# Kernel optimization log

Hardware: AMD Instinct MI355X
Metric: run time of the kernel (lower is better)

The kernel has to match this reference:

```python
import jax, jax.numpy as jnp
import numpy as np

TEMP = 1.0  # routing_temperature

def _gelu(x):
    return jax.nn.gelu(x, approximate=False)  # torch nn.GELU default (erf)

def setup_inputs() -> dict:
    key = jax.random.key(0)
    ks = jax.random.split(key, 6)
    B, S, D, E, I = 8, 2048, 768, 8, 3072
    H = I // 2
    def xav(k, shape):
        fan_in, fan_out = shape[-2], shape[-1]
        lim = float(np.sqrt(6.0 / (fan_in + fan_out)))
        return jax.random.uniform(k, shape, jnp.float32, -lim, lim)
    return {
        "x":  jax.random.normal(ks[0], (B, S, D), jnp.float32),
        "Wr": xav(ks[1], (D, E)),
        "br": jnp.zeros((E,), jnp.float32),
        "W1": xav(ks[2], (E, D, I)), "b1": jnp.zeros((E, I), jnp.float32),
        "W2": xav(ks[3], (E, I, H)), "b2": jnp.zeros((E, H), jnp.float32),
        "W3": xav(ks[4], (E, H, D)), "b3": jnp.zeros((E, D), jnp.float32),
        "top_k": 2,
    }

def reference(x, Wr, br, W1, b1, W2, b2, W3, b3, top_k):
    B, S, D = x.shape
    E = Wr.shape[1]
    T = B * S
    xt = x.reshape(T, D)                              # flatten tokens
    logits = (xt @ Wr + br) / TEMP                    # [T, E]
    vals, sel = jax.lax.top_k(logits, top_k)          # [T, k]
    w = jax.nn.softmax(vals, axis=-1)                 # softmax over top-k scores
    # dense per-token combine weights (zero for unselected experts)
    combine = jnp.zeros((T, E), x.dtype).at[jnp.arange(T)[:, None], sel].add(w)
    def step(acc, p):
        W1e, b1e, W2e, b2e, W3e, b3e, ce = p
        h = _gelu(xt @ W1e + b1e)                     # [T, I]
        h = _gelu(h @ W2e + b2e)                      # [T, I//2]
        y = h @ W3e + b3e                             # [T, D]
        return acc + ce[:, None] * y, None
    acc0 = jnp.zeros((T, D), x.dtype)
    out, _ = jax.lax.scan(step, acc0, (W1, b1, W2, b2, W3, b3, combine.T))
    return out.reshape(B, S, D)
```

## Files before the change

kernel.cpp:

```cpp
#include <hip/hip_runtime.h>
#include <hip/hip_fp16.h>
#include <cstdint>
#include <cstddef>

#define TK 16384
#define DD 768
#define EE 8
#define II 3072
#define HH 1536

typedef _Float16 half8 __attribute__((ext_vector_type(8)));
typedef float floatx4 __attribute__((ext_vector_type(4)));

typedef const __attribute__((address_space(1))) uint32_t* gptr_t;
typedef __attribute__((address_space(3))) uint32_t* lptr_t;

#define GLOAD_LDS16(gp, lp) __builtin_amdgcn_global_load_lds( \
    (gptr_t)(const void*)(gp), (lptr_t)(void*)(lp), 16, 0, 0)

__device__ inline void xcd_swizzle(int& e, int& m, int& n) {
  int gx = gridDim.x, gy = gridDim.y;
  int f = (blockIdx.z * gy + blockIdx.y) * gx + blockIdx.x;
  int xcd = f & 7, idx = f >> 3;
  int chunk = idx / gx, pos = idx - chunk * gx;
  int logical = chunk * (8 * gx) + xcd * gx + pos;
  int mn = gy * gx;
  e = logical / mn;
  int rem = logical - e * mn;
  m = rem / gx;
  n = rem - m * gx;
}

__global__ __launch_bounds__(256)
void cvtT_kernel(const float* __restrict__ in, __half* __restrict__ out,
                 int K, int N) {
  __shared__ float tile[64][65];
  int e = blockIdx.z;
  const float* inp = in + (size_t)e * K * N + (size_t)(blockIdx.y * 64) * N + blockIdx.x * 64;
  __half* outp = out + (size_t)e * K * N + (size_t)(blockIdx.x * 64) * K + blockIdx.y * 64;
  int s = threadIdx.x;
  int tx = s & 15, r0 = s >> 4;
#pragma unroll
  for (int i = 0; i < 4; ++i) {
    int k = r0 + i * 16;
    float4 v = *(const float4*)&inp[(size_t)k * N + tx * 4];
    tile[k][tx * 4 + 0] = v.x;
    tile[k][tx * 4 + 1] = v.y;
    tile[k][tx * 4 + 2] = v.z;
    tile[k][tx * 4 + 3] = v.w;
  }
  __syncthreads();
  int kp = s & 31;
#pragma unroll
  for (int i = 0; i < 8; ++i) {
    int n = (s >> 5) + i * 8;
    __half2 h = __floats2half2_rn(tile[2 * kp][n], tile[2 * kp + 1][n]);
    *(__half2*)&outp[(size_t)n * K + kp * 2] = h;
  }
}

__global__ __launch_bounds__(256)
void router_kernel(const float* __restrict__ x, const float* __restrict__ Wr,
                   const float* __restrict__ br, int* __restrict__ counts,
                   int* __restrict__ sel, float* __restrict__ wTok,
                   __half* __restrict__ xh) {
  __shared__ float wr_s[EE * DD];
  for (int i = threadIdx.x; i < EE * DD; i += 256) {
    int d = i >> 3, e = i & 7;
    wr_s[e * DD + d] = Wr[i];
  }
  __syncthreads();
  int wid = threadIdx.x >> 6, lane = threadIdx.x & 63;
  int t = blockIdx.x * 4 + wid;
  const float* xt = x + (size_t)t * DD;
  float acc[EE];
#pragma unroll
  for (int e = 0; e < EE; ++e) acc[e] = 0.f;
  for (int d = lane; d < DD; d += 64) {
    float xv = xt[d];
#pragma unroll
    for (int e = 0; e < EE; ++e) acc[e] += xv * wr_s[e * DD + d];
  }
#pragma unroll
  for (int off = 32; off > 0; off >>= 1)
#pragma unroll
    for (int e = 0; e < EE; ++e) acc[e] += __shfl_xor(acc[e], off);
  if (lane == 0) {
    float v[EE];
#pragma unroll
    for (int e = 0; e < EE; ++e) v[e] = acc[e] + br[e];
    int i0 = 0;
#pragma unroll
    for (int e = 1; e < EE; ++e) if (v[e] > v[i0]) i0 = e;
    int i1 = (i0 == 0) ? 1 : 0;
#pragma unroll
    for (int e = 0; e < EE; ++e) if (e != i0 && v[e] > v[i1] && e != i1) { if (v[e] > v[i1]) i1 = e; }
    float e1 = __expf(v[i1] - v[i0]);
    float s = 1.f / (1.f + e1);
    sel[2 * t] = i0; sel[2 * t + 1] = i1;
    wTok[2 * t] = s; wTok[2 * t + 1] = e1 * s;
    atomicAdd(&counts[i0], 1);
    atomicAdd(&counts[i1], 1);
  }
  const float4* xr = (const float4*)xt;
  uint2* xo = (uint2*)(xh + (size_t)t * DD);
#pragma unroll
  for (int j = 0; j < 3; ++j) {
    float4 v = xr[lane + j * 64];
    __half2 a = __floats2half2_rn(v.x, v.y);
    __half2 b = __floats2half2_rn(v.z, v.w);
    uint2 p;
    p.x = *(const unsigned int*)&a;
    p.y = *(const unsigned int*)&b;
    xo[lane + j * 64] = p;
  }
}

__global__ void offsets_kernel(const int* __restrict__ counts, int* __restrict__ offsets,
                               int* __restrict__ cursors) {
  if (threadIdx.x == 0) {
    int o = 0;
    for (int e = 0; e < EE; ++e) { offsets[e] = o; cursors[e] = o; o += counts[e]; }
  }
}

__global__ void scatter_kernel(const int* __restrict__ sel, int* __restrict__ cursors,
                               int* __restrict__ idxList, int* __restrict__ posTok) {
  int t = blockIdx.x * 256 + threadIdx.x;
  if (t < TK) {
#pragma unroll
    for (int k = 0; k < 2; ++k) {
      int e = sel[2 * t + k];
      int p = atomicAdd(&cursors[e], 1);
      idxList[p] = t;
      posTok[2 * t + k] = p;
    }
  }
}

template<int KD, int ND, bool GATHER, bool GELU>
__global__ __launch_bounds__(512, 1)
void ffn_gemm8(const __half* __restrict__ A, const __half* __restrict__ Wt,
               const float* __restrict__ Bias, __half* __restrict__ Out,
               const int* __restrict__ counts, const int* __restrict__ offsets,
               const int* __restrict__ idxList) {
  constexpr int NT = KD / 64;
  int e, mblk, nblk;
  xcd_swizzle(e, mblk, nblk);
  const int cnt = counts[e];
  const int m0 = mblk * 256;
  if (cnt == 0 || m0 >= cnt) return;
  const int off = offsets[e];
  const int n0 = nblk * 256;
  const __half* We = Wt + (size_t)e * KD * ND;
  const float* be = Bias + (size_t)e * ND;

  __shared__ __align__(16) __half As[2][256 * 64];
  __shared__ __align__(16) __half Bs[2][256 * 64];

  const int tid = threadIdx.x;
  const int srow = tid >> 3;
  const int swz = ((tid & 7) ^ (srow & 7)) << 3;

  const __half* aptr[4];
  const __half* bptr[4];
#pragma unroll
  for (int q = 0; q < 4; ++q) {
    int gr = m0 + q * 64 + srow;
    if (gr > cnt - 1) gr = cnt - 1;
    size_t arow = GATHER ? (size_t)idxList[off + gr] : (size_t)(off + gr);
    aptr[q] = A + arow * KD + swz;
    bptr[q] = We + (size_t)(n0 + q * 64 + srow) * KD + swz;
  }

#define STAGE_A(BUF, Q, TS) GLOAD_LDS16(aptr[Q] + (TS) * 64, &As[BUF][(Q) * 4096 + tid * 8])
#define STAGE_B(BUF, Q, TS) GLOAD_LDS16(bptr[Q] + (TS) * 64, &Bs[BUF][(Q) * 4096 + tid * 8])

  const int lane = tid & 63, wv = tid >> 6;
  const int wr = wv >> 2, wc = wv & 3;
  const int lrow = lane & 15, lg = lane >> 4;
  const int rowa = wr * 128 + lrow;
  const int rowb = wc * 64 + lrow;
  int aoff[2], boff[2];
#pragma unroll
  for (int kk = 0; kk < 2; ++kk) {
    aoff[kk] = rowa * 64 + (((kk * 4 + lg) ^ (rowa & 7)) << 3);
    boff[kk] = rowb * 64 + (((kk * 4 + lg) ^ (rowb & 7)) << 3);
  }

  floatx4 acc[8][4];
#pragma unroll
  for (int mi = 0; mi < 8; ++mi)
#pragma unroll
    for (int ni = 0; ni < 4; ++ni) acc[mi][ni] = (floatx4){0.f, 0.f, 0.f, 0.f};

#pragma unroll
  for (int q = 0; q < 4; ++q) STAGE_A(0, q, 0);
#pragma unroll
  for (int q = 0; q < 4; ++q) STAGE_B(0, q, 0);
#pragma unroll
  for (int q = 0; q < 4; ++q) STAGE_A(1, q, 1);
  STAGE_B(1, 0, 1);
  STAGE_B(1, 1, 1);
  asm volatile("s_waitcnt vmcnt(6)" ::: "memory");
  __builtin_amdgcn_s_barrier();

#define BAR() __builtin_amdgcn_s_barrier()
#define WLG() do { asm volatile("s_waitcnt lgkmcnt(0)" ::: "memory"); \
                   __builtin_amdgcn_sched_barrier(0); } while (0)
#define P1() __builtin_amdgcn_s_setprio(1)
#define P0() __builtin_amdgcn_s_setprio(0)
#define MMQ(AF, BF, MB, NB) \
  _Pragma("unroll") for (int kk = 0; kk < 2; ++kk) \
  _Pragma("unroll") for (int mi = 0; mi < 4; ++mi) \
  _Pragma("unroll") for (int ni = 0; ni < 2; ++ni) \
    acc[(MB) + mi][(NB) + ni] = __builtin_amdgcn_mfma_f32_16x16x32_f16( \
        AF[mi][kk], BF[ni][kk], acc[(MB) + mi][(NB) + ni], 0, 0, 0);

#define PHASES(CUR, NXT, TT) { \
  const __half* Ac = &As[CUR][0]; \
  const __half* Bc = &Bs[CUR][0]; \
  half8 af[4][2], bf0[2][2], bf1[2][2]; \
  _Pragma("unroll") for (int mi = 0; mi < 4; ++mi) \
  _Pragma("unroll") for (int kk = 0; kk < 2; ++kk) \
    af[mi][kk] = *(const half8*)&Ac[aoff[kk] + mi * 1024]; \
  _Pragma("unroll") for (int ni = 0; ni < 2; ++ni) \
  _Pragma("unroll") for (int kk = 0; kk < 2; ++kk) \
    bf0[ni][kk] = *(const half8*)&Bc[boff[kk] + ni * 1024]; \
  if ((TT) + 1 < NT) { STAGE_B(NXT, 2, (TT) + 1); STAGE_B(NXT, 3, (TT) + 1); } \
  BAR(); WLG(); P1(); MMQ(af, bf0, 0, 0); P0(); BAR(); \
  _Pragma("unroll") for (int ni = 0; ni < 2; ++ni) \
  _Pragma("unroll") for (int kk = 0; kk < 2; ++kk) \
    bf1[ni][kk] = *(const half8*)&Bc[boff[kk] + (ni + 2) * 1024]; \
  if ((TT) + 2 < NT) { STAGE_A(CUR, 0, (TT) + 2); STAGE_A(CUR, 2, (TT) + 2); } \
  BAR(); WLG(); P1(); MMQ(af, bf1, 0, 2); P0(); BAR(); \
  _Pragma("unroll") for (int mi = 0; mi < 4; ++mi) \
  _Pragma("unroll") for (int kk = 0; kk < 2; ++kk) \
    af[mi][kk] = *(const half8*)&Ac[aoff[kk] + (mi + 4) * 1024]; \
  if ((TT) + 2 < NT) { STAGE_B(CUR, 0, (TT) + 2); STAGE_B(CUR, 1, (TT) + 2); } \
  BAR(); WLG(); P1(); MMQ(af, bf0, 4, 0); P0(); BAR(); \
  if ((TT) + 2 < NT) { STAGE_A(CUR, 1, (TT) + 2); STAGE_A(CUR, 3, (TT) + 2); } \
  BAR(); P1(); MMQ(af, bf1, 4, 2); P0(); \
  if ((TT) + 2 < NT) { asm volatile("s_waitcnt vmcnt(6)" ::: "memory"); } \
  else              { asm volatile("s_waitcnt vmcnt(0)" ::: "memory"); } \
  BAR(); }

  for (int t = 0; t < NT; t += 2) {
    PHASES(0, 1, t)
    PHASES(1, 0, t + 1)
  }

  const int crow = m0 + wr * 128 + lg * 4;
  const int ccol = n0 + wc * 64 + lrow;
  float bv[4];
#pragma unroll
  for (int ni = 0; ni < 4; ++ni) bv[ni] = be[ccol + ni * 16];
#pragma unroll
  for (int mi = 0; mi < 8; ++mi) {
#pragma unroll
    for (int j = 0; j < 4; ++j) {
      int r = crow + mi * 16 + j;
      if (r < cnt) {
#pragma unroll
        for (int ni = 0; ni < 4; ++ni) {
          float v = acc[mi][ni][j] + bv[ni];
          if (GELU) v = 0.5f * v * (1.f + erff(v * 0.70710678118654752f));
          Out[(size_t)(off + r) * ND + ccol + ni * 16] = __float2half(v);
        }
      }
    }
  }
#undef STAGE_A
#undef STAGE_B
#undef BAR
#undef WLG
#undef P1
#undef P0
#undef MMQ
#undef PHASES
}

__global__ void combine_kernel(const __half* __restrict__ yc, const float* __restrict__ wTok,
                               const int* __restrict__ posTok, float* __restrict__ out) {
  int t = blockIdx.x;
  int d = threadIdx.x * 4;
  if (d >= DD) return;
  float w0 = wTok[2 * t], w1 = wTok[2 * t + 1];
  const __half2* a = (const __half2*)(yc + (size_t)posTok[2 * t] * DD + d);
  const __half2* b = (const __half2*)(yc + (size_t)posTok[2 * t + 1] * DD + d);
  float2 a0 = __half22float2(a[0]), a1 = __half22float2(a[1]);
  float2 b0 = __half22float2(b[0]), b1 = __half22float2(b[1]);
  float4 r;
  r.x = w0 * a0.x + w1 * b0.x;
  r.y = w0 * a0.y + w1 * b0.y;
  r.z = w0 * a1.x + w1 * b1.x;
  r.w = w0 * a1.y + w1 * b1.y;
  *(float4*)(out + (size_t)t * DD + d) = r;
}

extern "C" void kernel_launch(void* const* d_in, const int* in_sizes, int n_in,
                              void* d_out, int out_size, void* d_ws, size_t ws_size,
                              hipStream_t stream) {
  const float* x  = (const float*)d_in[0];
  const float* Wr = (const float*)d_in[1];
  const float* br = (const float*)d_in[2];
  const float* W1 = (const float*)d_in[3];
  const float* b1 = (const float*)d_in[4];
  const float* W2 = (const float*)d_in[5];
  const float* b2 = (const float*)d_in[6];
  const float* W3 = (const float*)d_in[7];
  const float* b3 = (const float*)d_in[8];
  float* out = (float*)d_out;

  char* ws = (char*)d_ws;
  size_t o = 0;
  auto alloc = [&](size_t bytes) {
    char* p = ws + o;
    o += (bytes + 255) & ~(size_t)255;
    return p;
  };
  __half* xh   = (__half*)alloc((size_t)TK * DD * 2);
  __half* w1t  = (__half*)alloc((size_t)EE * DD * II * 2);
  __half* w2t  = (__half*)alloc((size_t)EE * II * HH * 2);
  __half* w3t  = (__half*)alloc((size_t)EE * HH * DD * 2);
  __half* h1   = (__half*)alloc((size_t)2 * TK * II * 2);
  __half* h2   = (__half*)alloc((size_t)2 * TK * HH * 2);
  __half* yc   = (__half*)alloc((size_t)2 * TK * DD * 2);
  int*   idxL  = (int*)alloc(2 * TK * 4);
  int*   sel   = (int*)alloc(2 * TK * 4);
  float* wTok  = (float*)alloc(2 * TK * 4);
  int*   posT  = (int*)alloc(2 * TK * 4);
  int*   counts  = (int*)alloc(256);
  int*   offsets = (int*)alloc(256);
  int*   cursors = (int*)alloc(256);
  if (o > ws_size) return;

  hipMemsetAsync(counts, 0, 256, stream);

  cvtT_kernel<<<dim3(II / 64, DD / 64, EE), 256, 0, stream>>>(W1, w1t, DD, II);
  cvtT_kernel<<<dim3(HH / 64, II / 64, EE), 256, 0, stream>>>(W2, w2t, II, HH);
  cvtT_kernel<<<dim3(DD / 64, HH / 64, EE), 256, 0, stream>>>(W3, w3t, HH, DD);
  router_kernel<<<TK / 4, 256, 0, stream>>>(x, Wr, br, counts, sel, wTok, xh);
  offsets_kernel<<<1, 64, 0, stream>>>(counts, offsets, cursors);
  scatter_kernel<<<TK / 256, 256, 0, stream>>>(sel, cursors, idxL, posT);

  ffn_gemm8<DD, II, true,  true ><<<dim3(II / 256, 64, EE), 512, 0, stream>>>(
      xh, w1t, b1, h1, counts, offsets, idxL);
  ffn_gemm8<II, HH, false, true ><<<dim3(HH / 256, 64, EE), 512, 0, stream>>>(
      h1, w2t, b2, h2, counts, offsets, idxL);
  ffn_gemm8<HH, DD, false, false><<<dim3(DD / 256, 64, EE), 512, 0, stream>>>(
      h2, w3t, b3, yc, counts, offsets, idxL);

  combine_kernel<<<TK, 192, 0, stream>>>(yc, wTok, posT, out);
}
```

Baseline: 1.505 ms.

## Load all A fragments up front and reverse block order in second GEMM

The GEMM phase schedule now reads all eight A fragments from LDS at the start of each k-tile rather than in two halves. Because of that, all four A stage loads for tile t+2 can be issued earlier, and one wait-and-barrier point is dropped. The second FFN GEMM also walks its blocks in reverse order, which may let it start on data the first GEMM just wrote while it is still in cache, and may balance the tail. The price is more registers for the A fragments under a 512-thread, 1-wave launch bound, which could cause spills.

```diff
diff --git a/kernel.cpp b/kernel.cpp
--- a/kernel.cpp
+++ b/kernel.cpp
@@ -18,9 +18,10 @@
 #define GLOAD_LDS16(gp, lp) __builtin_amdgcn_global_load_lds( \
     (gptr_t)(const void*)(gp), (lptr_t)(void*)(lp), 16, 0, 0)
 
-__device__ inline void xcd_swizzle(int& e, int& m, int& n) {
+__device__ inline void xcd_swizzle(int& e, int& m, int& n, bool rev) {
   int gx = gridDim.x, gy = gridDim.y;
   int f = (blockIdx.z * gy + blockIdx.y) * gx + blockIdx.x;
+  if (rev) f = gx * gy * 8 - 1 - f;
   int xcd = f & 7, idx = f >> 3;
   int chunk = idx / gx, pos = idx - chunk * gx;
   int logical = chunk * (8 * gx) + xcd * gx + pos;
@@ -138,7 +139,7 @@
   }
 }
 
-template<int KD, int ND, bool GATHER, bool GELU>
+template<int KD, int ND, bool GATHER, bool GELU, bool REV>
 __global__ __launch_bounds__(512, 1)
 void ffn_gemm8(const __half* __restrict__ A, const __half* __restrict__ Wt,
                const float* __restrict__ Bias, __half* __restrict__ Out,
@@ -146,7 +147,7 @@
                const int* __restrict__ idxList) {
   constexpr int NT = KD / 64;
   int e, mblk, nblk;
-  xcd_swizzle(e, mblk, nblk);
+  xcd_swizzle(e, mblk, nblk, REV);
   const int cnt = counts[e];
   const int m0 = mblk * 256;
   if (cnt == 0 || m0 >= cnt) return;
@@ -210,37 +211,38 @@
                    __builtin_amdgcn_sched_barrier(0); } while (0)
 #define P1() __builtin_amdgcn_s_setprio(1)
 #define P0() __builtin_amdgcn_s_setprio(0)
-#define MMQ(AF, BF, MB, NB) \
+#define MMQ(AO, BF, MB, NB) \
   _Pragma("unroll") for (int kk = 0; kk < 2; ++kk) \
   _Pragma("unroll") for (int mi = 0; mi < 4; ++mi) \
   _Pragma("unroll") for (int ni = 0; ni < 2; ++ni) \
     acc[(MB) + mi][(NB) + ni] = __builtin_amdgcn_mfma_f32_16x16x32_f16( \
-        AF[mi][kk], BF[ni][kk], acc[(MB) + mi][(NB) + ni], 0, 0, 0);
+        af[(AO) + mi][kk], BF[ni][kk], acc[(MB) + mi][(NB) + ni], 0, 0, 0);
 
 #define PHASES(CUR, NXT, TT) { \
   const __half* Ac = &As[CUR][0]; \
   const __half* Bc = &Bs[CUR][0]; \
-  half8 af[4][2], bf0[2][2], bf1[2][2]; \
-  _Pragma("unroll") for (int mi = 0; mi < 4; ++mi) \
+  half8 af[8][2], bf0[2][2], bf1[2][2]; \
+   \
+  _Pragma("unroll") for (int mi = 0; mi < 8; ++mi) \
   _Pragma("unroll") for (int kk = 0; kk < 2; ++kk) \
     af[mi][kk] = *(const half8*)&Ac[aoff[kk] + mi * 1024]; \
   _Pragma("unroll") for (int ni = 0; ni < 2; ++ni) \
   _Pragma("unroll") for (int kk = 0; kk < 2; ++kk) \
     bf0[ni][kk] = *(const half8*)&Bc[boff[kk] + ni * 1024]; \
   if ((TT) + 1 < NT) { STAGE_B(NXT, 2, (TT) + 1); STAGE_B(NXT, 3, (TT) + 1); } \
-  BAR(); WLG(); P1(); MMQ(af, bf0, 0, 0); P0(); BAR(); \
+  BAR(); WLG(); P1(); MMQ(0, bf0, 0, 0); P0(); BAR(); \
+   \
   _Pragma("unroll") for (int ni = 0; ni < 2; ++ni) \
   _Pragma("unroll") for (int kk = 0; kk < 2; ++kk) \
     bf1[ni][kk] = *(const half8*)&Bc[boff[kk] + (ni + 2) * 1024]; \
-  if ((TT) + 2 < NT) { STAGE_A(CUR, 0, (TT) + 2); STAGE_A(CUR, 2, (TT) + 2); } \
-  BAR(); WLG(); P1(); MMQ(af, bf1, 0, 2); P0(); BAR(); \
-  _Pragma("unroll") for (int mi = 0; mi < 4; ++mi) \
-  _Pragma("unroll") for (int kk = 0; kk < 2; ++kk) \
-    af[mi][kk] = *(const half8*)&Ac[aoff[kk] + (mi + 4) * 1024]; \
+  if ((TT) + 2 < NT) { STAGE_A(CUR, 0, (TT) + 2); STAGE_A(CUR, 1, (TT) + 2); \
+                       STAGE_A(CUR, 2, (TT) + 2); STAGE_A(CUR, 3, (TT) + 2); } \
+  BAR(); WLG(); P1(); MMQ(0, bf1, 0, 2); P0(); BAR(); \
+   \
   if ((TT) + 2 < NT) { STAGE_B(CUR, 0, (TT) + 2); STAGE_B(CUR, 1, (TT) + 2); } \
-  BAR(); WLG(); P1(); MMQ(af, bf0, 4, 0); P0(); BAR(); \
-  if ((TT) + 2 < NT) { STAGE_A(CUR, 1, (TT) + 2); STAGE_A(CUR, 3, (TT) + 2); } \
-  BAR(); P1(); MMQ(af, bf1, 4, 2); P0(); \
+  BAR(); P1(); MMQ(4, bf0, 4, 0); P0(); BAR(); \
+   \
+  P1(); MMQ(4, bf1, 4, 2); P0(); \
   if ((TT) + 2 < NT) { asm volatile("s_waitcnt vmcnt(6)" ::: "memory"); } \
   else              { asm volatile("s_waitcnt vmcnt(0)" ::: "memory"); } \
   BAR(); }
@@ -344,11 +346,11 @@
   offsets_kernel<<<1, 64, 0, stream>>>(counts, offsets, cursors);
   scatter_kernel<<<TK / 256, 256, 0, stream>>>(sel, cursors, idxL, posT);
 
-  ffn_gemm8<DD, II, true,  true ><<<dim3(II / 256, 64, EE), 512, 0, stream>>>(
+  ffn_gemm8<DD, II, true,  true,  false><<<dim3(II / 256, 64, EE), 512, 0, stream>>>(
       xh, w1t, b1, h1, counts, offsets, idxL);
-  ffn_gemm8<II, HH, false, true ><<<dim3(HH / 256, 64, EE), 512, 0, stream>>>(
+  ffn_gemm8<II, HH, false, true,  true ><<<dim3(HH / 256, 64, EE), 512, 0, stream>>>(
       h1, w2t, b2, h2, counts, offsets, idxL);
-  ffn_gemm8<HH, DD, false, false><<<dim3(DD / 256, 64, EE), 512, 0, stream>>>(
+  ffn_gemm8<HH, DD, false, false, false><<<dim3(DD / 256, 64, EE), 512, 0, stream>>>(
       h2, w3t, b3, yc, counts, offsets, idxL);
 
   combine_kernel<<<TK, 192, 0, stream>>>(yc, wTok, posT, out);
```

Result: slower. 2.190 ms (+45.5%).

## Triple-buffer A tiles in LDS and prefetch whole A tile two steps ahead

Applied to the files above, without the earlier changes.

The A operand moves from double to triple buffering in shared memory. All four A sub-tiles for step t+2 are now issued at the start of each phase, and the main loop is unrolled by six to rotate the buffer indices. A separate fragment register set for the second half of A lets one barrier between the last two MFMA groups be dropped. The aim is earlier, less fragmented global-to-LDS loads and fewer syncs. The cost is LDS growing to about 160KB, the full budget, plus higher VGPR pressure.

```diff
diff --git a/kernel.cpp b/kernel.cpp
--- a/kernel.cpp
+++ b/kernel.cpp
@@ -155,7 +155,7 @@
   const __half* We = Wt + (size_t)e * KD * ND;
   const float* be = Bias + (size_t)e * ND;
 
-  __shared__ __align__(16) __half As[2][256 * 64];
+  __shared__ __align__(16) __half As[3][256 * 64];
   __shared__ __align__(16) __half Bs[2][256 * 64];
 
   const int tid = threadIdx.x;
@@ -195,13 +195,13 @@
     for (int ni = 0; ni < 4; ++ni) acc[mi][ni] = (floatx4){0.f, 0.f, 0.f, 0.f};
 
 #pragma unroll
+  for (int q = 0; q < 4; ++q) STAGE_B(0, q, 0);
+#pragma unroll
   for (int q = 0; q < 4; ++q) STAGE_A(0, q, 0);
-#pragma unroll
-  for (int q = 0; q < 4; ++q) STAGE_B(0, q, 0);
-#pragma unroll
-  for (int q = 0; q < 4; ++q) STAGE_A(1, q, 1);
   STAGE_B(1, 0, 1);
   STAGE_B(1, 1, 1);
+#pragma unroll
+  for (int q = 0; q < 4; ++q) STAGE_A(1, q, 1);
   asm volatile("s_waitcnt vmcnt(6)" ::: "memory");
   __builtin_amdgcn_s_barrier();
 
@@ -217,37 +217,45 @@
     acc[(MB) + mi][(NB) + ni] = __builtin_amdgcn_mfma_f32_16x16x32_f16( \
         AF[mi][kk], BF[ni][kk], acc[(MB) + mi][(NB) + ni], 0, 0, 0);
 
-#define PHASES(CUR, NXT, TT) { \
-  const __half* Ac = &As[CUR][0]; \
-  const __half* Bc = &Bs[CUR][0]; \
-  half8 af[4][2], bf0[2][2], bf1[2][2]; \
+#define PHASES(AC, AN2, BC, BN, TT) { \
+  const __half* Ac = &As[AC][0]; \
+  const __half* Bc = &Bs[BC][0]; \
+  half8 af[4][2], ag[4][2], bf0[2][2], bf1[2][2]; \
+   \
   _Pragma("unroll") for (int mi = 0; mi < 4; ++mi) \
   _Pragma("unroll") for (int kk = 0; kk < 2; ++kk) \
     af[mi][kk] = *(const half8*)&Ac[aoff[kk] + mi * 1024]; \
   _Pragma("unroll") for (int ni = 0; ni < 2; ++ni) \
   _Pragma("unroll") for (int kk = 0; kk < 2; ++kk) \
     bf0[ni][kk] = *(const half8*)&Bc[boff[kk] + ni * 1024]; \
-  if ((TT) + 1 < NT) { STAGE_B(NXT, 2, (TT) + 1); STAGE_B(NXT, 3, (TT) + 1); } \
+  if ((TT) + 1 < NT) { STAGE_B(BN, 2, (TT) + 1); STAGE_B(BN, 3, (TT) + 1); } \
+  if ((TT) + 2 < NT) { STAGE_A(AN2, 0, (TT) + 2); STAGE_A(AN2, 1, (TT) + 2); \
+                       STAGE_A(AN2, 2, (TT) + 2); STAGE_A(AN2, 3, (TT) + 2); } \
   BAR(); WLG(); P1(); MMQ(af, bf0, 0, 0); P0(); BAR(); \
+   \
   _Pragma("unroll") for (int ni = 0; ni < 2; ++ni) \
   _Pragma("unroll") for (int kk = 0; kk < 2; ++kk) \
     bf1[ni][kk] = *(const half8*)&Bc[boff[kk] + (ni + 2) * 1024]; \
-  if ((TT) + 2 < NT) { STAGE_A(CUR, 0, (TT) + 2); STAGE_A(CUR, 2, (TT) + 2); } \
   BAR(); WLG(); P1(); MMQ(af, bf1, 0, 2); P0(); BAR(); \
+   \
   _Pragma("unroll") for (int mi = 0; mi < 4; ++mi) \
   _Pragma("unroll") for (int kk = 0; kk < 2; ++kk) \
-    af[mi][kk] = *(const half8*)&Ac[aoff[kk] + (mi + 4) * 1024]; \
-  if ((TT) + 2 < NT) { STAGE_B(CUR, 0, (TT) + 2); STAGE_B(CUR, 1, (TT) + 2); } \
-  BAR(); WLG(); P1(); MMQ(af, bf0, 4, 0); P0(); BAR(); \
-  if ((TT) + 2 < NT) { STAGE_A(CUR, 1, (TT) + 2); STAGE_A(CUR, 3, (TT) + 2); } \
-  BAR(); P1(); MMQ(af, bf1, 4, 2); P0(); \
+    ag[mi][kk] = *(const half8*)&Ac[aoff[kk] + (mi + 4) * 1024]; \
+  if ((TT) + 2 < NT) { STAGE_B(BC, 0, (TT) + 2); STAGE_B(BC, 1, (TT) + 2); } \
+  BAR(); WLG(); P1(); MMQ(ag, bf0, 4, 0); P0(); BAR(); \
+   \
+  P1(); MMQ(ag, bf1, 4, 2); P0(); \
   if ((TT) + 2 < NT) { asm volatile("s_waitcnt vmcnt(6)" ::: "memory"); } \
   else              { asm volatile("s_waitcnt vmcnt(0)" ::: "memory"); } \
   BAR(); }
 
-  for (int t = 0; t < NT; t += 2) {
-    PHASES(0, 1, t)
-    PHASES(1, 0, t + 1)
+  for (int t = 0; t < NT; t += 6) {
+    PHASES(0, 2, 0, 1, t)
+    PHASES(1, 0, 1, 0, t + 1)
+    PHASES(2, 1, 0, 1, t + 2)
+    PHASES(0, 2, 1, 0, t + 3)
+    PHASES(1, 0, 0, 1, t + 4)
+    PHASES(2, 1, 1, 0, t + 5)
   }
 
   const int crow = m0 + wr * 128 + lg * 4;
```

Measured after the change: 1.918 ms. +27.4%, slower.
